# Performance work log

Measured on AMD Instinct MI355X. Metric: run time of the kernel, lower is better.

## Reference

```python
import jax, jax.numpy as jnp
import numpy as np

B, L, D, C, NB = 2, 256, 3, 256, 64
LN_EPS = 1e-5


def setup_inputs() -> dict:
    ks = jax.random.split(jax.random.key(0), 12)
    x_BLD = jax.random.normal(ks[0], (B, L, D), dtype=jnp.float32) * 0.5
    c_BD = jax.random.normal(ks[1], (B, C), dtype=jnp.float32)
    embed_w = jax.random.normal(ks[2], (NB, C), dtype=jnp.float32) * 0.02
    pos_w = jax.random.normal(ks[3], (128, C), dtype=jnp.float32) * 0.02
    bins = jnp.linspace(0.0, 3.0, NB - 1, dtype=jnp.float32)
    ada_w = jax.random.normal(ks[4], (3 * C, C), dtype=jnp.float32) * (C ** -0.5)
    ada_b = jnp.zeros((3 * C,), dtype=jnp.float32)
    ln_g = jnp.ones((C,), dtype=jnp.float32)
    ln_b = jnp.zeros((C,), dtype=jnp.float32)
    fc1_w = jax.random.normal(ks[5], (4 * C, C), dtype=jnp.float32) * (C ** -0.5)
    fc1_b = jnp.zeros((4 * C,), dtype=jnp.float32)
    fc2_w = jax.random.normal(ks[6], (C, 4 * C), dtype=jnp.float32) * ((4 * C) ** -0.5)
    fc2_b = jnp.zeros((C,), dtype=jnp.float32)
    return {"x_BLD": x_BLD, "c_BD": c_BD, "embed_w": embed_w, "pos_w": pos_w,
            "bins": bins, "ada_w": ada_w, "ada_b": ada_b, "ln_g": ln_g,
            "ln_b": ln_b, "fc1_w": fc1_w, "fc1_b": fc1_b, "fc2_w": fc2_w,
            "fc2_b": fc2_b}


def reference(x_BLD, c_BD, embed_w, pos_w, bins, ada_w, ada_b, ln_g, ln_b,
              fc1_w, fc1_b, fc2_w, fc2_b):
    # pairwise squared distances: [B, L, L]
    d_BLL = jnp.sum((x_BLD[:, :, None, :] - x_BLD[:, None, :, :]) ** 2, axis=-1)
    # bucketize (torch.bucketize right=False == searchsorted side='left')
    idx_BLL = jnp.searchsorted(bins, d_BLL, side="left")
    # relative position embedding: [L, L, C]
    rel = jnp.arange(L)[:, None] - jnp.arange(L)[None, :]
    rel = jnp.clip(rel, -64, 63) + 64
    pos_LLD = pos_w[rel]
    # adaLN modulation from conditioning: SiLU -> Linear -> 3 chunks
    mod = jax.nn.silu(c_BD) @ ada_w.T + ada_b            # [B, 3C]
    shift, scale, gate = jnp.split(mod, 3, axis=-1)      # each [B, C]
    shift = shift[:, None, None, :]
    scale = scale[:, None, None, :]
    gate = gate[:, None, None, :]
    # embed + pos, affine modulate
    s = embed_w[idx_BLL] + pos_LLD[None]                 # [B, L, L, C]
    s = s * (1.0 + scale) + shift
    # LayerNorm over channel dim
    mu = jnp.mean(s, axis=-1, keepdims=True)
    var = jnp.mean((s - mu) ** 2, axis=-1, keepdims=True)
    h = (s - mu) * jax.lax.rsqrt(var + LN_EPS) * ln_g + ln_b
    # MLP: Linear -> GELU(exact) -> Linear
    h = jax.nn.gelu(h @ fc1_w.T + fc1_b, approximate=False)
    h = h @ fc2_w.T + fc2_b
    return s + gate * h
```

## Files before the change

### kernel.cpp

```cpp
#include <hip/hip_runtime.h>
#include <math.h>

#define Cn 256
#define Ln 256
#define Bn 2
#define H1 1024
#define NIDX 64
#define NREL 128
#define NCOMBO 16384
#define TROWS 32

typedef __attribute__((ext_vector_type(8))) short bf16x8;
typedef __attribute__((ext_vector_type(4))) float f32x4;
typedef unsigned int u32;

__device__ __forceinline__ float gelu_exact(float x) {
    return 0.5f * x * (1.0f + erff(x * 0.70710678118654752f));
}
__device__ __forceinline__ short f2bf(float f) {
    unsigned u = __float_as_uint(f);
    return (short)((u + 0x7fffu + ((u >> 16) & 1u)) >> 16);
}

__global__ __launch_bounds__(256) void prep_kernel(
    const float* __restrict__ c_BD, const float* __restrict__ ada_w,
    const float* __restrict__ ada_b, const float* __restrict__ fc1_w,
    const float* __restrict__ fc2_w, float* __restrict__ mod,
    short* __restrict__ fc1bf, short* __restrict__ fc2bf)
{
    const int bid = blockIdx.x;
    const int tid = threadIdx.x;
    if (bid < 512) {
        const int N = Cn * H1;
        int i = (bid * 256 + tid) * 4;
        const float* s;
        short* d;
        if (i < N) { s = fc1_w + i; d = fc1bf + i; }
        else       { s = fc2_w + (i - N); d = fc2bf + (i - N); }
        float4 v = *(const float4*)s;
        short4 o;
        o.x = f2bf(v.x); o.y = f2bf(v.y); o.z = f2bf(v.z); o.w = f2bf(v.w);
        *(short4*)d = o;
    } else {
        int o = (bid - 512) * 256 + tid;
        int b = o / (3 * Cn);
        int j = o - b * (3 * Cn);
        const float* crow = c_BD + b * Cn;
        const float* wrow = ada_w + (size_t)j * Cn;
        float acc = 0.f;
        for (int k = 0; k < Cn; k += 4) {
            float4 cv = *(const float4*)(crow + k);
            float4 wv = *(const float4*)(wrow + k);
            acc += (cv.x / (1.f + expf(-cv.x))) * wv.x;
            acc += (cv.y / (1.f + expf(-cv.y))) * wv.y;
            acc += (cv.z / (1.f + expf(-cv.z))) * wv.z;
            acc += (cv.w / (1.f + expf(-cv.w))) * wv.w;
        }
        mod[o] = acc + ada_b[j];
    }
}

__global__ __launch_bounds__(512, 4) void table_fused_kernel(
    const float* __restrict__ embed_w, const float* __restrict__ pos_w,
    const float* __restrict__ ln_g, const float* __restrict__ ln_b,
    const short* __restrict__ fc1bf, const float* __restrict__ fc1_b,
    const short* __restrict__ fc2bf, const float* __restrict__ fc2_b,
    const float* __restrict__ mod, float* __restrict__ table)
{
    __shared__ __align__(16) short h_lds[TROWS][264];
    __shared__ __align__(16) short g_lds[TROWS][264];

    const int tid  = threadIdx.x;
    const int wave = tid >> 6;
    const int lane = tid & 63;
    const int quad = lane >> 4;
    const int l15  = lane & 15;

    const int base = blockIdx.x * TROWS;
    const int b    = base >> 13;
    const int idx  = (base >> 7) & 63;
    const int rel0 = base & 127;

    const float* modb = mod + b * (3 * Cn);
    const float* erow = embed_w + (size_t)idx * Cn;

    {
        const int c0 = lane * 4;
        float4 ev = *(const float4*)(erow + c0);
        float4 sc = *(const float4*)(modb + Cn + c0);
        sc.x += 1.f; sc.y += 1.f; sc.z += 1.f; sc.w += 1.f;
        const float4 sh = *(const float4*)(modb + c0);
        const float4 lg = *(const float4*)(ln_g + c0);
        const float4 lb = *(const float4*)(ln_b + c0);
        #pragma unroll
        for (int r4 = 0; r4 < 4; ++r4) {
            const int rr = wave * 4 + r4;
            const float4 p = *(const float4*)(pos_w + (size_t)(rel0 + rr) * Cn + c0);
            float v0 = (ev.x + p.x) * sc.x + sh.x;
            float v1 = (ev.y + p.y) * sc.y + sh.y;
            float v2 = (ev.z + p.z) * sc.z + sh.z;
            float v3 = (ev.w + p.w) * sc.w + sh.w;
            float sum = v0 + v1 + v2 + v3;
            #pragma unroll
            for (int off = 32; off; off >>= 1) sum += __shfl_xor(sum, off, 64);
            const float mu = sum * (1.f / Cn);
            float t0 = v0 - mu, t1 = v1 - mu, t2 = v2 - mu, t3 = v3 - mu;
            float p2 = t0 * t0 + t1 * t1 + t2 * t2 + t3 * t3;
            #pragma unroll
            for (int off = 32; off; off >>= 1) p2 += __shfl_xor(p2, off, 64);
            const float rstd = rsqrtf(p2 * (1.f / Cn) + 1e-5f);
            short4 hq;
            hq.x = f2bf(t0 * rstd * lg.x + lb.x);
            hq.y = f2bf(t1 * rstd * lg.y + lb.y);
            hq.z = f2bf(t2 * rstd * lg.z + lb.z);
            hq.w = f2bf(t3 * rstd * lg.w + lb.w);
            *(short4*)(&h_lds[rr][c0]) = hq;
        }
    }
    __syncthreads();

    f32x4 acc2[2][2];
    #pragma unroll
    for (int mt = 0; mt < 2; ++mt)
        #pragma unroll
        for (int nt = 0; nt < 2; ++nt) acc2[mt][nt] = (f32x4){0.f, 0.f, 0.f, 0.f};

    for (int c = 0; c < 4; ++c) {
        f32x4 z[2][2];
        #pragma unroll
        for (int mt = 0; mt < 2; ++mt)
            #pragma unroll
            for (int nt = 0; nt < 2; ++nt) z[mt][nt] = (f32x4){0.f, 0.f, 0.f, 0.f};

        {
            const short* w1base = fc1bf + (size_t)(c * 256 + wave * 32 + l15) * Cn + quad * 8;
            bf16x8 wA[4][2], wB[4][2];
            #pragma unroll
            for (int ks = 0; ks < 4; ++ks)
                #pragma unroll
                for (int nt = 0; nt < 2; ++nt)
                    wA[ks][nt] = *(const bf16x8*)(w1base + nt * 16 * Cn + ks * 32);
            #pragma unroll
            for (int ks = 0; ks < 4; ++ks)
                #pragma unroll
                for (int nt = 0; nt < 2; ++nt)
                    wB[ks][nt] = *(const bf16x8*)(w1base + nt * 16 * Cn + (ks + 4) * 32);
            #pragma unroll
            for (int ks = 0; ks < 4; ++ks) {
                const int k0 = ks * 32 + quad * 8;
                bf16x8 a0 = *(const bf16x8*)(&h_lds[l15][k0]);
                bf16x8 a1 = *(const bf16x8*)(&h_lds[16 + l15][k0]);
                #pragma unroll
                for (int nt = 0; nt < 2; ++nt) {
                    z[0][nt] = __builtin_amdgcn_mfma_f32_16x16x32_bf16(wA[ks][nt], a0, z[0][nt], 0, 0, 0);
                    z[1][nt] = __builtin_amdgcn_mfma_f32_16x16x32_bf16(wA[ks][nt], a1, z[1][nt], 0, 0, 0);
                }
            }
            #pragma unroll
            for (int ks = 0; ks < 4; ++ks) {
                const int k0 = (ks + 4) * 32 + quad * 8;
                bf16x8 a0 = *(const bf16x8*)(&h_lds[l15][k0]);
                bf16x8 a1 = *(const bf16x8*)(&h_lds[16 + l15][k0]);
                #pragma unroll
                for (int nt = 0; nt < 2; ++nt) {
                    z[0][nt] = __builtin_amdgcn_mfma_f32_16x16x32_bf16(wB[ks][nt], a0, z[0][nt], 0, 0, 0);
                    z[1][nt] = __builtin_amdgcn_mfma_f32_16x16x32_bf16(wB[ks][nt], a1, z[1][nt], 0, 0, 0);
                }
            }
        }
        __syncthreads();

        #pragma unroll
        for (int mt = 0; mt < 2; ++mt) {
            #pragma unroll
            for (int nt = 0; nt < 2; ++nt) {
                const int cc = wave * 32 + nt * 16 + quad * 4;
                const float4 b4 = *(const float4*)(fc1_b + c * 256 + cc);
                short4 o;
                o.x = f2bf(gelu_exact(z[mt][nt][0] + b4.x));
                o.y = f2bf(gelu_exact(z[mt][nt][1] + b4.y));
                o.z = f2bf(gelu_exact(z[mt][nt][2] + b4.z));
                o.w = f2bf(gelu_exact(z[mt][nt][3] + b4.w));
                *(short4*)(&g_lds[mt * 16 + l15][cc]) = o;
            }
        }
        __syncthreads();

        {
            const short* w2base = fc2bf + (size_t)(wave * 32 + l15) * H1 + c * 256 + quad * 8;
            bf16x8 wA[4][2], wB[4][2];
            #pragma unroll
            for (int ks = 0; ks < 4; ++ks)
                #pragma unroll
                for (int nt = 0; nt < 2; ++nt)
                    wA[ks][nt] = *(const bf16x8*)(w2base + nt * 16 * H1 + ks * 32);
            #pragma unroll
            for (int ks = 0; ks < 4; ++ks)
                #pragma unroll
                for (int nt = 0; nt < 2; ++nt)
                    wB[ks][nt] = *(const bf16x8*)(w2base + nt * 16 * H1 + (ks + 4) * 32);
            #pragma unroll
            for (int ks = 0; ks < 4; ++ks) {
                const int k0 = ks * 32 + quad * 8;
                bf16x8 a0 = *(const bf16x8*)(&g_lds[l15][k0]);
                bf16x8 a1 = *(const bf16x8*)(&g_lds[16 + l15][k0]);
                #pragma unroll
                for (int nt = 0; nt < 2; ++nt) {
                    acc2[0][nt] = __builtin_amdgcn_mfma_f32_16x16x32_bf16(wA[ks][nt], a0, acc2[0][nt], 0, 0, 0);
                    acc2[1][nt] = __builtin_amdgcn_mfma_f32_16x16x32_bf16(wA[ks][nt], a1, acc2[1][nt], 0, 0, 0);
                }
            }
            #pragma unroll
            for (int ks = 0; ks < 4; ++ks) {
                const int k0 = (ks + 4) * 32 + quad * 8;
                bf16x8 a0 = *(const bf16x8*)(&g_lds[l15][k0]);
                bf16x8 a1 = *(const bf16x8*)(&g_lds[16 + l15][k0]);
                #pragma unroll
                for (int nt = 0; nt < 2; ++nt) {
                    acc2[0][nt] = __builtin_amdgcn_mfma_f32_16x16x32_bf16(wB[ks][nt], a0, acc2[0][nt], 0, 0, 0);
                    acc2[1][nt] = __builtin_amdgcn_mfma_f32_16x16x32_bf16(wB[ks][nt], a1, acc2[1][nt], 0, 0, 0);
                }
            }
        }
        if (c < 3) __syncthreads();
    }

    #pragma unroll
    for (int mt = 0; mt < 2; ++mt) {
        const int row = mt * 16 + l15;
        const float* prow = pos_w + (size_t)(rel0 + row) * Cn;
        #pragma unroll
        for (int nt = 0; nt < 2; ++nt) {
            const int n0 = wave * 32 + nt * 16 + quad * 4;
            const float4 b4 = *(const float4*)(fc2_b + n0);
            const float4 g4 = *(const float4*)(modb + 2 * Cn + n0);
            const float4 sc = *(const float4*)(modb + Cn + n0);
            const float4 sh = *(const float4*)(modb + n0);
            const float4 e4 = *(const float4*)(erow + n0);
            const float4 p4 = *(const float4*)(prow + n0);
            float4 o;
            float s;
            s   = (e4.x + p4.x) * (1.f + sc.x) + sh.x;
            o.x = s + g4.x * (acc2[mt][nt][0] + b4.x);
            s   = (e4.y + p4.y) * (1.f + sc.y) + sh.y;
            o.y = s + g4.y * (acc2[mt][nt][1] + b4.y);
            s   = (e4.z + p4.z) * (1.f + sc.z) + sh.z;
            o.z = s + g4.z * (acc2[mt][nt][2] + b4.z);
            s   = (e4.w + p4.w) * (1.f + sc.w) + sh.w;
            o.w = s + g4.w * (acc2[mt][nt][3] + b4.w);
            *(float4*)(table + (size_t)(base + row) * Cn + n0) = o;
        }
    }
}

__global__ __launch_bounds__(256) void gather_kernel(
    const float* __restrict__ x, const float* __restrict__ bins,
    const float* __restrict__ table, float* __restrict__ out)
{
    __shared__ float xs[Ln * 3];
    __shared__ float bins_s[63];
    __shared__ int   idx_s[64];

    const int tid = threadIdx.x;
    const int blk = blockIdx.x;
    const int q   = blk & 3;
    const int bi  = blk >> 2;
    const int b   = bi >> 8;
    const int i   = bi & 255;

    for (int t = tid; t < Ln * 3; t += 256) xs[t] = x[(size_t)b * Ln * 3 + t];
    if (tid < 63) bins_s[tid] = bins[tid];
    __syncthreads();

    if (tid < 64) {
        int j = q * 64 + tid;
        float d0 = xs[3 * i]     - xs[3 * j];
        float d1 = xs[3 * i + 1] - xs[3 * j + 1];
        float d2 = xs[3 * i + 2] - xs[3 * j + 2];
        float d = d0 * d0 + d1 * d1 + d2 * d2;
        int v = 0;
        #pragma unroll
        for (int k = 0; k < 63; ++k) v += (bins_s[k] < d) ? 1 : 0;
        idx_s[tid] = v;
    }
    __syncthreads();

    const int wave = tid >> 6;
    const int lane = tid & 63;
    float4* outp = (float4*)(out + (size_t)bi * Ln * Cn);
    const float4* tab4 = (const float4*)table;

    float4 v[16];
    #pragma unroll
    for (int jj = 0; jj < 16; ++jj) {
        int jl  = wave * 16 + jj;
        int j   = q * 64 + jl;
        int rel = i - j;
        rel = (rel < -64 ? -64 : (rel > 63 ? 63 : rel)) + 64;
        size_t trow = (size_t)((b * NIDX + idx_s[jl]) * NREL + rel) * (Cn / 4);
        v[jj] = tab4[trow + lane];
    }
    #pragma unroll
    for (int jj = 0; jj < 16; ++jj) {
        int j = q * 64 + wave * 16 + jj;
        outp[(size_t)j * (Cn / 4) + lane] = v[jj];
    }
}

extern "C" void kernel_launch(void* const* d_in, const int* in_sizes, int n_in,
                              void* d_out, int out_size, void* d_ws, size_t ws_size,
                              hipStream_t stream) {
    const float* x_BLD   = (const float*)d_in[0];
    const float* c_BD    = (const float*)d_in[1];
    const float* embed_w = (const float*)d_in[2];
    const float* pos_w   = (const float*)d_in[3];
    const float* bins    = (const float*)d_in[4];
    const float* ada_w   = (const float*)d_in[5];
    const float* ada_b   = (const float*)d_in[6];
    const float* ln_g    = (const float*)d_in[7];
    const float* ln_b    = (const float*)d_in[8];
    const float* fc1_w   = (const float*)d_in[9];
    const float* fc1_b   = (const float*)d_in[10];
    const float* fc2_w   = (const float*)d_in[11];
    const float* fc2_b   = (const float*)d_in[12];
    float* out = (float*)d_out;

    char* ws = (char*)d_ws;
    float* mod   = (float*)ws;
    short* fc1bf = (short*)(ws + 8192);
    short* fc2bf = (short*)(ws + 8192 + 524288);
    float* table = (float*)(ws + 8192 + 2 * 524288);

    prep_kernel<<<518, 256, 0, stream>>>(c_BD, ada_w, ada_b, fc1_w, fc2_w,
                                         mod, fc1bf, fc2bf);
    table_fused_kernel<<<NCOMBO / TROWS, 512, 0, stream>>>(
        embed_w, pos_w, ln_g, ln_b, fc1bf, fc1_b, fc2bf, fc2_b, mod, table);
    gather_kernel<<<Bn * Ln * 4, 256, 0, stream>>>(x_BLD, bins, table, out);
}
```

Baseline: 268.6 us.

## Pre-swizzle bf16 MLP weights into MFMA fragment order for coalesced loads

The prep kernel now writes the fc1 and fc2 bf16 weights in per-wave, per-k-step fragment order, so each 64-lane wave reads one contiguous 1 KB chunk per MFMA operand. Before, each lane read strided 16-byte pieces from row-major weight rows. The table kernel's weight-fragment loads become fully coalesced and the two half-unrolled load/compute loops merge into one 8-step loop. The cost is a more complex index mapping in prep and more registers held live at once (16 fragments).

```diff
diff --git a/kernel.cpp b/kernel.cpp
--- a/kernel.cpp
+++ b/kernel.cpp
@@ -26,23 +26,42 @@
     const float* __restrict__ c_BD, const float* __restrict__ ada_w,
     const float* __restrict__ ada_b, const float* __restrict__ fc1_w,
     const float* __restrict__ fc2_w, float* __restrict__ mod,
-    short* __restrict__ fc1bf, short* __restrict__ fc2bf)
+    short* __restrict__ fc1s, short* __restrict__ fc2s)
 {
     const int bid = blockIdx.x;
     const int tid = threadIdx.x;
-    if (bid < 512) {
-        const int N = Cn * H1;
-        int i = (bid * 256 + tid) * 4;
-        const float* s;
-        short* d;
-        if (i < N) { s = fc1_w + i; d = fc1bf + i; }
-        else       { s = fc2_w + (i - N); d = fc2bf + (i - N); }
-        float4 v = *(const float4*)s;
-        short4 o;
-        o.x = f2bf(v.x); o.y = f2bf(v.y); o.z = f2bf(v.z); o.w = f2bf(v.w);
-        *(short4*)d = o;
+    if (bid < 128) {
+        const int t   = bid * 256 + tid;
+        const int row = t >> 5;
+        const int cc  = t & 31;
+        const int c   = row >> 8, wv = (row >> 5) & 7, nt = (row >> 4) & 1, l15 = row & 15;
+        const int ks  = cc >> 2, quad = cc & 3;
+        const int lane = quad * 16 + l15;
+        const int u   = (c * 8 + wv) * 16 + nt * 8 + ks;
+        const float* s = fc1_w + (size_t)row * Cn + cc * 8;
+        float4 v0 = *(const float4*)s;
+        float4 v1 = *(const float4*)(s + 4);
+        bf16x8 o;
+        o[0] = f2bf(v0.x); o[1] = f2bf(v0.y); o[2] = f2bf(v0.z); o[3] = f2bf(v0.w);
+        o[4] = f2bf(v1.x); o[5] = f2bf(v1.y); o[6] = f2bf(v1.z); o[7] = f2bf(v1.w);
+        *(bf16x8*)(fc1s + (size_t)u * 512 + lane * 8) = o;
+    } else if (bid < 256) {
+        const int t   = (bid - 128) * 256 + tid;
+        const int row = t >> 7;
+        const int cc  = t & 127;
+        const int wv  = (row >> 5) & 7, nt = (row >> 4) & 1, l15 = row & 15;
+        const int c   = cc >> 5, ks = (cc >> 2) & 7, quad = cc & 3;
+        const int lane = quad * 16 + l15;
+        const int u   = (c * 8 + wv) * 16 + nt * 8 + ks;
+        const float* s = fc2_w + (size_t)row * H1 + cc * 8;
+        float4 v0 = *(const float4*)s;
+        float4 v1 = *(const float4*)(s + 4);
+        bf16x8 o;
+        o[0] = f2bf(v0.x); o[1] = f2bf(v0.y); o[2] = f2bf(v0.z); o[3] = f2bf(v0.w);
+        o[4] = f2bf(v1.x); o[5] = f2bf(v1.y); o[6] = f2bf(v1.z); o[7] = f2bf(v1.w);
+        *(bf16x8*)(fc2s + (size_t)u * 512 + lane * 8) = o;
     } else {
-        int o = (bid - 512) * 256 + tid;
+        int o = (bid - 256) * 256 + tid;
         int b = o / (3 * Cn);
         int j = o - b * (3 * Cn);
         const float* crow = c_BD + b * Cn;
@@ -63,8 +82,8 @@
 __global__ __launch_bounds__(512, 4) void table_fused_kernel(
     const float* __restrict__ embed_w, const float* __restrict__ pos_w,
     const float* __restrict__ ln_g, const float* __restrict__ ln_b,
-    const short* __restrict__ fc1bf, const float* __restrict__ fc1_b,
-    const short* __restrict__ fc2bf, const float* __restrict__ fc2_b,
+    const short* __restrict__ fc1s, const float* __restrict__ fc1_b,
+    const short* __restrict__ fc2s, const float* __restrict__ fc2_b,
     const float* __restrict__ mod, float* __restrict__ table)
 {
     __shared__ __align__(16) short h_lds[TROWS][264];
@@ -133,38 +152,22 @@
             for (int nt = 0; nt < 2; ++nt) z[mt][nt] = (f32x4){0.f, 0.f, 0.f, 0.f};
 
         {
-            const short* w1base = fc1bf + (size_t)(c * 256 + wave * 32 + l15) * Cn + quad * 8;
-            bf16x8 wA[4][2], wB[4][2];
-            #pragma unroll
-            for (int ks = 0; ks < 4; ++ks)
+            const short* w1u = fc1s + (size_t)((c * 8 + wave) * 16) * 512 + lane * 8;
+            bf16x8 wf[8][2];
+            #pragma unroll
+            for (int ks = 0; ks < 8; ++ks)
                 #pragma unroll
                 for (int nt = 0; nt < 2; ++nt)
-                    wA[ks][nt] = *(const bf16x8*)(w1base + nt * 16 * Cn + ks * 32);
-            #pragma unroll
-            for (int ks = 0; ks < 4; ++ks)
-                #pragma unroll
-                for (int nt = 0; nt < 2; ++nt)
-                    wB[ks][nt] = *(const bf16x8*)(w1base + nt * 16 * Cn + (ks + 4) * 32);
-            #pragma unroll
-            for (int ks = 0; ks < 4; ++ks) {
+                    wf[ks][nt] = *(const bf16x8*)(w1u + (nt * 8 + ks) * 512);
+            #pragma unroll
+            for (int ks = 0; ks < 8; ++ks) {
                 const int k0 = ks * 32 + quad * 8;
                 bf16x8 a0 = *(const bf16x8*)(&h_lds[l15][k0]);
                 bf16x8 a1 = *(const bf16x8*)(&h_lds[16 + l15][k0]);
                 #pragma unroll
                 for (int nt = 0; nt < 2; ++nt) {
-                    z[0][nt] = __builtin_amdgcn_mfma_f32_16x16x32_bf16(wA[ks][nt], a0, z[0][nt], 0, 0, 0);
-                    z[1][nt] = __builtin_amdgcn_mfma_f32_16x16x32_bf16(wA[ks][nt], a1, z[1][nt], 0, 0, 0);
-                }
-            }
-            #pragma unroll
-            for (int ks = 0; ks < 4; ++ks) {
-                const int k0 = (ks + 4) * 32 + quad * 8;
-                bf16x8 a0 = *(const bf16x8*)(&h_lds[l15][k0]);
-                bf16x8 a1 = *(const bf16x8*)(&h_lds[16 + l15][k0]);
-                #pragma unroll
-                for (int nt = 0; nt < 2; ++nt) {
-                    z[0][nt] = __builtin_amdgcn_mfma_f32_16x16x32_bf16(wB[ks][nt], a0, z[0][nt], 0, 0, 0);
-                    z[1][nt] = __builtin_amdgcn_mfma_f32_16x16x32_bf16(wB[ks][nt], a1, z[1][nt], 0, 0, 0);
+                    z[0][nt] = __builtin_amdgcn_mfma_f32_16x16x32_bf16(wf[ks][nt], a0, z[0][nt], 0, 0, 0);
+                    z[1][nt] = __builtin_amdgcn_mfma_f32_16x16x32_bf16(wf[ks][nt], a1, z[1][nt], 0, 0, 0);
                 }
             }
         }
@@ -187,38 +190,22 @@
         __syncthreads();
 
         {
-            const short* w2base = fc2bf + (size_t)(wave * 32 + l15) * H1 + c * 256 + quad * 8;
-            bf16x8 wA[4][2], wB[4][2];
-            #pragma unroll
-            for (int ks = 0; ks < 4; ++ks)
+            const short* w2u = fc2s + (size_t)((c * 8 + wave) * 16) * 512 + lane * 8;
+            bf16x8 wf[8][2];
+            #pragma unroll
+            for (int ks = 0; ks < 8; ++ks)
                 #pragma unroll
                 for (int nt = 0; nt < 2; ++nt)
-                    wA[ks][nt] = *(const bf16x8*)(w2base + nt * 16 * H1 + ks * 32);
-            #pragma unroll
-            for (int ks = 0; ks < 4; ++ks)
-                #pragma unroll
-                for (int nt = 0; nt < 2; ++nt)
-                    wB[ks][nt] = *(const bf16x8*)(w2base + nt * 16 * H1 + (ks + 4) * 32);
-            #pragma unroll
-            for (int ks = 0; ks < 4; ++ks) {
+                    wf[ks][nt] = *(const bf16x8*)(w2u + (nt * 8 + ks) * 512);
+            #pragma unroll
+            for (int ks = 0; ks < 8; ++ks) {
                 const int k0 = ks * 32 + quad * 8;
                 bf16x8 a0 = *(const bf16x8*)(&g_lds[l15][k0]);
                 bf16x8 a1 = *(const bf16x8*)(&g_lds[16 + l15][k0]);
                 #pragma unroll
                 for (int nt = 0; nt < 2; ++nt) {
-                    acc2[0][nt] = __builtin_amdgcn_mfma_f32_16x16x32_bf16(wA[ks][nt], a0, acc2[0][nt], 0, 0, 0);
-                    acc2[1][nt] = __builtin_amdgcn_mfma_f32_16x16x32_bf16(wA[ks][nt], a1, acc2[1][nt], 0, 0, 0);
-                }
-            }
-            #pragma unroll
-            for (int ks = 0; ks < 4; ++ks) {
-                const int k0 = (ks + 4) * 32 + quad * 8;
-                bf16x8 a0 = *(const bf16x8*)(&g_lds[l15][k0]);
-                bf16x8 a1 = *(const bf16x8*)(&g_lds[16 + l15][k0]);
-                #pragma unroll
-                for (int nt = 0; nt < 2; ++nt) {
-                    acc2[0][nt] = __builtin_amdgcn_mfma_f32_16x16x32_bf16(wB[ks][nt], a0, acc2[0][nt], 0, 0, 0);
-                    acc2[1][nt] = __builtin_amdgcn_mfma_f32_16x16x32_bf16(wB[ks][nt], a1, acc2[1][nt], 0, 0, 0);
+                    acc2[0][nt] = __builtin_amdgcn_mfma_f32_16x16x32_bf16(wf[ks][nt], a0, acc2[0][nt], 0, 0, 0);
+                    acc2[1][nt] = __builtin_amdgcn_mfma_f32_16x16x32_bf16(wf[ks][nt], a1, acc2[1][nt], 0, 0, 0);
                 }
             }
         }
@@ -327,13 +314,13 @@
 
     char* ws = (char*)d_ws;
     float* mod   = (float*)ws;
-    short* fc1bf = (short*)(ws + 8192);
-    short* fc2bf = (short*)(ws + 8192 + 524288);
+    short* fc1s  = (short*)(ws + 8192);
+    short* fc2s  = (short*)(ws + 8192 + 524288);
     float* table = (float*)(ws + 8192 + 2 * 524288);
 
-    prep_kernel<<<518, 256, 0, stream>>>(c_BD, ada_w, ada_b, fc1_w, fc2_w,
-                                         mod, fc1bf, fc2bf);
+    prep_kernel<<<262, 256, 0, stream>>>(c_BD, ada_w, ada_b, fc1_w, fc2_w,
+                                         mod, fc1s, fc2s);
     table_fused_kernel<<<NCOMBO / TROWS, 512, 0, stream>>>(
-        embed_w, pos_w, ln_g, ln_b, fc1bf, fc1_b, fc2bf, fc2_b, mod, table);
+        embed_w, pos_w, ln_g, ln_b, fc1s, fc1_b, fc2s, fc2_b, mod, table);
     gather_kernel<<<Bn * Ln * 4, 256, 0, stream>>>(x_BLD, bins, table, out);
 }
```

After: 239.9 us. 1.12x faster.
